# Optimization experiments

Hardware: AMD Instinct MI355X
Metric: run time of the kernel (lower is better)

Reference implementation:

```python
import jax, jax.numpy as jnp
import numpy as np
import math

D_MODEL = 1152
D_K = 1152
NUM_HEADS = 8
HEAD_DIM = D_K // NUM_HEADS  # 144
SIGMA = 2.0
EPS = 1e-6


def rope_2d(keys, positions):
    # keys: [B, N, D]; positions: [B, N, 2] float (x, y)
    B, N, D = keys.shape
    half = D // 2
    quarter = D // 4
    idx = jnp.arange(quarter, dtype=keys.dtype)
    theta = 1.0 / (10000.0 ** (2.0 * idx / half))  # [quarter]
    fx = positions[..., 0][..., None] * theta  # [B, N, quarter]
    fy = positions[..., 1][..., None] * theta

    def apply_rope(part, f):
        p = part.reshape(B, N, quarter, 2)
        c, s = jnp.cos(f), jnp.sin(f)
        o1 = p[..., 0] * c - p[..., 1] * s
        o2 = p[..., 0] * s + p[..., 1] * c
        return jnp.stack([o1, o2], axis=-1).reshape(B, N, half)

    return jnp.concatenate(
        [apply_rope(keys[..., :half], fx), apply_rope(keys[..., half:], fy)], axis=-1
    )


def layernorm_nobias(x, w, eps=EPS):
    mu = jnp.mean(x, axis=-1, keepdims=True)
    var = jnp.mean(jnp.square(x - mu), axis=-1, keepdims=True)
    return (x - mu) * jax.lax.rsqrt(var + eps) * w


def setup_inputs() -> dict:
    key = jax.random.key(0)
    ks = jax.random.split(key, 9)
    T, HW, M = 64, 729, 512
    features = jax.random.normal(ks[0], (T, HW, D_MODEL), dtype=jnp.float32)
    tracks = jax.random.uniform(ks[1], (T, M, 2), dtype=jnp.float32) * 27.0
    track_tokens = jax.random.normal(ks[2], (T, M, D_MODEL), dtype=jnp.float32)
    feature_positions = jax.random.uniform(ks[3], (HW, 2), dtype=jnp.float32) * 27.0
    sc = 1.0 / math.sqrt(D_MODEL)
    # weights stored [in, out]; torch Linear computes x @ W.T with W [out, in]
    W_q = jax.random.normal(ks[4], (D_MODEL, D_K), dtype=jnp.float32) * sc
    W_k = jax.random.normal(ks[5], (D_MODEL, D_K), dtype=jnp.float32) * sc
    q_norm_w = jnp.ones((D_K,), dtype=jnp.float32)
    k_norm_w = jnp.ones((D_K,), dtype=jnp.float32)
    out_proj_w = jax.random.normal(ks[6], (D_MODEL, D_MODEL), dtype=jnp.float32) * sc
    return {
        "features": features,
        "tracks": tracks,
        "track_tokens": track_tokens,
        "feature_positions": feature_positions,
        "W_q": W_q,
        "W_k": W_k,
        "q_norm_w": q_norm_w,
        "k_norm_w": k_norm_w,
        "out_proj_w": out_proj_w,
    }


def reference(features, tracks, track_tokens, feature_positions,
              W_q, W_k, q_norm_w, k_norm_w, out_proj_w):
    T, HW, _ = features.shape
    M = tracks.shape[1]
    Q = track_tokens @ W_q  # [T, M, d_k]
    K = features @ W_k      # [T, HW, d_k]
    feat_pos = jnp.broadcast_to(feature_positions[None], (T, HW, 2))
    K = rope_2d(K, feat_pos)
    Q = layernorm_nobias(Q, q_norm_w)
    K = layernorm_nobias(K, k_norm_w)
    Qh = Q.reshape(T, M, NUM_HEADS, HEAD_DIM).transpose(0, 2, 1, 3)   # [T,H,M,dh]
    Kh = K.reshape(T, HW, NUM_HEADS, HEAD_DIM).transpose(0, 2, 1, 3)  # [T,H,HW,dh]
    Vh = features.reshape(T, HW, NUM_HEADS, -1).transpose(0, 2, 1, 3) # [T,H,HW,dv]
    scores = jnp.einsum("thmd,thnd->thmn", Qh, Kh) / math.sqrt(HEAD_DIM)
    # Gaussian spatial bias: -||track - feat||^2 / (2 sigma^2), shared across heads
    diff = tracks[:, :, None, :] - feature_positions[None, None, :, :]  # [T,M,HW,2]
    dist2 = jnp.sum(jnp.square(diff), axis=-1)  # [T,M,HW]
    bias = -dist2 / (2.0 * SIGMA ** 2)
    scores = scores + bias[:, None, :, :]
    attn = jax.nn.softmax(scores, axis=-1)
    sampled = jnp.einsum("thmn,thnd->thmd", attn, Vh)  # [T,H,M,dv]
    sampled = sampled.transpose(0, 2, 1, 3).reshape(T, M, -1)
    return sampled @ out_proj_w
```

## Files before the change

kernel.cpp:

```cpp
#include <hip/hip_runtime.h>
#include <hip/hip_bf16.h>
#include <math.h>

typedef float f32x4 __attribute__((ext_vector_type(4)));
typedef __bf16 bf16x8 __attribute__((ext_vector_type(8)));

#define T_N 64
#define HW_N 729
#define HW_P 736
#define M_N 512
#define DM 1152
#define NH 8
#define DH 144
#define MQ 32768
#define MK 46656
#define MK_PAD 46720

#define SZ_FEAT ((size_t)MK_PAD * DM * 2)
#define SZ_VT   ((size_t)T_N * NH * DH * HW_P * 2)
#define SZ_OV   (SZ_VT > SZ_FEAT ? SZ_VT : SZ_FEAT)
#define SZ_Q    ((size_t)MQ * DM * 2)
#define SZ_W    ((size_t)DM * DM * 2)
#define OFF_KN   ((size_t)0)
#define OFF_TOK  (OFF_KN + SZ_FEAT)
#define OFF_QN   (OFF_TOK + SZ_Q)
#define OFF_OV   (OFF_QN + SZ_Q)
#define OFF_WT   (OFF_OV + SZ_OV)
#define WS_NEED  (OFF_WT + 3 * SZ_W)

__device__ __forceinline__ void async_copy16(void* lds, const void* g) {
    __builtin_amdgcn_global_load_lds(
        (const __attribute__((address_space(1))) void*)g,
        (__attribute__((address_space(3))) void*)lds, 16, 0, 0);
}

__global__ __launch_bounds__(256) void cvt_bf16(const float* __restrict__ src,
                                                __bf16* __restrict__ dst,
                                                long valid4, long total4) {
    long i = (long)blockIdx.x * 256 + threadIdx.x;
    if (i >= total4) return;
    float4 f = {0.f, 0.f, 0.f, 0.f};
    if (i < valid4) f = ((const float4*)src)[i];
    __bf16 tmp[4] = {(__bf16)f.x, (__bf16)f.y, (__bf16)f.z, (__bf16)f.w};
    *((uint2*)(dst + i * 4)) = *((uint2*)tmp);
}

__global__ __launch_bounds__(256) void transpose_w(const float* __restrict__ W,
                                                   __bf16* __restrict__ Wt) {
    __shared__ float tile[32][33];
    const int k0 = blockIdx.x * 32, n0 = blockIdx.y * 32;
    const int tx = threadIdx.x, ty = threadIdx.y;
    #pragma unroll
    for (int i = 0; i < 32; i += 8)
        tile[ty + i][tx] = W[(long)(k0 + ty + i) * DM + n0 + tx];
    __syncthreads();
    #pragma unroll
    for (int i = 0; i < 32; i += 8)
        Wt[(long)(n0 + ty + i) * DM + k0 + tx] = (__bf16)tile[tx][ty + i];
}

__global__ __launch_bounds__(256) void transpose_v(const float* __restrict__ f,
                                                   __bf16* __restrict__ vt) {
    __shared__ float tile[32][149];
    const int hw0 = blockIdx.x * 32, h = blockIdx.y, t = blockIdx.z;
    const int tid = threadIdx.x;
    for (int c = tid; c < 32 * 36; c += 256) {
        const int r = c / 36, s = c % 36;
        const int hw = hw0 + r;
        float4 v = {0.f, 0.f, 0.f, 0.f};
        if (hw < HW_N) v = *(const float4*)(f + ((long)t * HW_N + hw) * DM + h * DH + s * 4);
        tile[r][s * 4 + 0] = v.x; tile[r][s * 4 + 1] = v.y;
        tile[r][s * 4 + 2] = v.z; tile[r][s * 4 + 3] = v.w;
    }
    __syncthreads();
    for (int c = tid; c < DH * 4; c += 256) {
        const int d = c >> 2, s = c & 3;
        __bf16 tmp[8];
        #pragma unroll
        for (int i = 0; i < 8; ++i) tmp[i] = (__bf16)tile[s * 8 + i][d];
        *(uint4*)(vt + ((long)(t * NH + h) * DH + d) * HW_P + hw0 + s * 8) = *(uint4*)tmp;
    }
}

template<bool STORE_BF16>
__global__ __launch_bounds__(256) void gemm_bt(const __bf16* __restrict__ A,
                                               const __bf16* __restrict__ Bt,
                                               void* __restrict__ Cout) {
    __shared__ __align__(16) __bf16 As[128 * 32];
    __shared__ __align__(16) __bf16 Bs[128 * 32];
    const int tid  = threadIdx.x;
    const int wave = tid >> 6, lane = tid & 63;
    const int quad = lane >> 4, l16 = lane & 15;
    const int wr = wave >> 1, wc = wave & 1;
    const long m0 = (long)blockIdx.x * 128;
    const long n0 = (long)blockIdx.y * 128;
    const int swzr = quad ^ ((l16 >> 1) & 3);
    f32x4 acc[4][4] = {};
    for (int kt = 0; kt < 36; ++kt) {
        const int k0 = kt * 32;
        __syncthreads();
        #pragma unroll
        for (int s = 0; s < 2; ++s) {
            const int c = s * 256 + tid;
            const int row = c >> 2;
            const int gkc = (c & 3) ^ ((c >> 3) & 3);
            async_copy16(As + c * 8, A  + (m0 + row) * DM + k0 + gkc * 8);
            async_copy16(Bs + c * 8, Bt + (n0 + row) * DM + k0 + gkc * 8);
        }
        __syncthreads();
        bf16x8 af[4], bfr[4];
        #pragma unroll
        for (int i = 0; i < 4; ++i)
            af[i] = *(const bf16x8*)(As + (wr * 64 + i * 16 + l16) * 32 + swzr * 8);
        #pragma unroll
        for (int j = 0; j < 4; ++j)
            bfr[j] = *(const bf16x8*)(Bs + (wc * 64 + j * 16 + l16) * 32 + swzr * 8);
        #pragma unroll
        for (int i = 0; i < 4; ++i)
            #pragma unroll
            for (int j = 0; j < 4; ++j)
                acc[i][j] = __builtin_amdgcn_mfma_f32_16x16x32_bf16(af[i], bfr[j], acc[i][j], 0, 0, 0);
    }
    #pragma unroll
    for (int i = 0; i < 4; ++i) {
        #pragma unroll
        for (int j = 0; j < 4; ++j) {
            #pragma unroll
            for (int r = 0; r < 4; ++r) {
                const long row = m0 + wr * 64 + i * 16 + quad * 4 + r;
                const long col = n0 + wc * 64 + j * 16 + l16;
                if constexpr (STORE_BF16)
                    ((__bf16*)Cout)[row * DM + col] = (__bf16)acc[i][j][r];
                else
                    ((float*)Cout)[row * DM + col] = acc[i][j][r];
            }
        }
    }
}

__global__ __launch_bounds__(256) void ln_q(__bf16* __restrict__ Q, const float* __restrict__ w) {
    const long row = blockIdx.x;
    __bf16* p = Q + row * DM;
    const int tid = threadIdx.x;
    float v[5];
    int nv = 0;
    float s = 0.f, s2 = 0.f;
    for (int i = tid; i < DM; i += 256) {
        float x = (float)p[i];
        v[nv++] = x; s += x; s2 += x * x;
    }
    #pragma unroll
    for (int o = 32; o > 0; o >>= 1) { s += __shfl_down(s, o); s2 += __shfl_down(s2, o); }
    __shared__ float red[8];
    if ((tid & 63) == 0) { red[tid >> 6] = s; red[4 + (tid >> 6)] = s2; }
    __syncthreads();
    const float S  = red[0] + red[1] + red[2] + red[3];
    const float S2 = red[4] + red[5] + red[6] + red[7];
    const float mu  = S * (1.f / DM);
    const float var = S2 * (1.f / DM) - mu * mu;
    const float rstd = rsqrtf(var + 1e-6f);
    nv = 0;
    for (int i = tid; i < DM; i += 256)
        p[i] = (__bf16)((v[nv++] - mu) * rstd * w[i]);
}

__global__ __launch_bounds__(256) void rope_ln_k(__bf16* __restrict__ K,
                                                 const float* __restrict__ fpos,
                                                 const float* __restrict__ w) {
    const long row = blockIdx.x;
    const int hw = (int)(row % HW_N);
    const float px = fpos[hw * 2 + 0];
    const float py = fpos[hw * 2 + 1];
    __bf16* p = K + row * DM;
    __shared__ float buf[DM];
    __shared__ float red[8];
    const int tid = threadIdx.x;
    float s = 0.f, s2 = 0.f;
    for (int pr = tid; pr < 576; pr += 256) {
        const bool isx = pr < 288;
        const int  i   = isx ? pr : pr - 288;
        const int  off = isx ? 2 * i : 576 + 2 * i;
        const float pos = isx ? px : py;
        const float theta = exp2f((float)i * -0.046137890206768924f);
        float sn, cs;
        sincosf(pos * theta, &sn, &cs);
        const float a = (float)p[off], b = (float)p[off + 1];
        const float o1 = a * cs - b * sn;
        const float o2 = a * sn + b * cs;
        buf[off] = o1; buf[off + 1] = o2;
        s += o1 + o2; s2 += o1 * o1 + o2 * o2;
    }
    #pragma unroll
    for (int o = 32; o > 0; o >>= 1) { s += __shfl_down(s, o); s2 += __shfl_down(s2, o); }
    if ((tid & 63) == 0) { red[tid >> 6] = s; red[4 + (tid >> 6)] = s2; }
    __syncthreads();
    const float S  = red[0] + red[1] + red[2] + red[3];
    const float S2 = red[4] + red[5] + red[6] + red[7];
    const float mu  = S * (1.f / DM);
    const float var = S2 * (1.f / DM) - mu * mu;
    const float rstd = rsqrtf(var + 1e-6f);
    for (int i = tid; i < DM; i += 256)
        p[i] = (__bf16)((buf[i] - mu) * rstd * w[i]);
}

__global__ __launch_bounds__(256, 3) void attn(const __bf16* __restrict__ Qn,
                                               const __bf16* __restrict__ Kn,
                                               const __bf16* __restrict__ Vt,
                                               const float* __restrict__ tracks,
                                               const float* __restrict__ fpos,
                                               __bf16* __restrict__ Out) {
    __shared__ __align__(16) __bf16 VtL[DH * 72];
    __shared__ __align__(16) __bf16 Ps[128 * 72];
    __shared__ float2 trkL[128];
    const int b  = blockIdx.x;
    const int qt = b & 3;
    const int th = b >> 2;
    const int h  = th & 7;
    const int t  = th >> 3;
    const int tid = threadIdx.x;
    const int wave = tid >> 6, lane = tid & 63;
    const int quad = lane >> 4, l16 = lane & 15;
    const int wq = wave * 32;

    if (tid < 128) trkL[tid] = ((const float2*)tracks)[(long)t * M_N + qt * 128 + tid];

    const __bf16* qb = Qn + ((long)t * M_N + qt * 128 + wq) * DM + h * DH;
    const __bf16* kb = Kn + (long)t * HW_N * DM + h * DH;
    const __bf16* vb = Vt + (long)(t * NH + h) * DH * HW_P;
    const __bf16* zpg = Kn + (size_t)MK * DM;

    f32x4 Ot[2][9] = {};
    float mrow[2][4], lrow[2][4];
    #pragma unroll
    for (int rt = 0; rt < 2; ++rt)
        #pragma unroll
        for (int r = 0; r < 4; ++r) { mrow[rt][r] = -1e30f; lrow[rt][r] = 0.f; }

    for (int kt = 0; kt < 12; ++kt) {
        const int kv0 = kt * 64;
        __syncthreads();
        for (int c = tid; c < DH * 9; c += 256) {
            const int r = c / 9, s = c % 9;
            const __bf16* g = (s < 8 && (kv0 + s * 8 + 8) <= HW_P)
                                ? vb + (long)r * HW_P + kv0 + s * 8 : zpg;
            async_copy16(VtL + c * 8, g);
        }
        __syncthreads();
        f32x4 sc[2][4] = {};
        #pragma unroll
        for (int kc = 0; kc < 5; ++kc) {
            bf16x8 aq[2];
            #pragma unroll
            for (int rt = 0; rt < 2; ++rt) {
                uint4 u = {0u, 0u, 0u, 0u};
                if (kc < 4 || quad < 2)
                    u = *(const uint4*)(qb + (long)(rt * 16 + l16) * DM + kc * 32 + quad * 8);
                aq[rt] = *(bf16x8*)&u;
            }
            #pragma unroll
            for (int jt = 0; jt < 4; ++jt) {
                const bf16x8 bk = *(const bf16x8*)(kb + (long)(kv0 + jt * 16 + l16) * DM + kc * 32 + quad * 8);
                #pragma unroll
                for (int rt = 0; rt < 2; ++rt)
                    sc[rt][jt] = __builtin_amdgcn_mfma_f32_16x16x32_bf16(aq[rt], bk, sc[rt][jt], 0, 0, 0);
            }
        }
        float fx[4], fy[4]; bool msk[4];
        #pragma unroll
        for (int jt = 0; jt < 4; ++jt) {
            const int kv = kv0 + jt * 16 + l16;
            msk[jt] = kv >= HW_N;
            float2 fp = {0.f, 0.f};
            if (!msk[jt]) fp = ((const float2*)fpos)[kv];
            fx[jt] = fp.x; fy[jt] = fp.y;
        }
        float alpha[2][4];
        #pragma unroll
        for (int rt = 0; rt < 2; ++rt) {
            #pragma unroll
            for (int r = 0; r < 4; ++r) {
                const int row = wq + rt * 16 + quad * 4 + r;
                const float tx = trkL[row].x, ty = trkL[row].y;
                float sv[4];
                float mx = -1e30f;
                #pragma unroll
                for (int jt = 0; jt < 4; ++jt) {
                    const float dx = tx - fx[jt], dy = ty - fy[jt];
                    float v = sc[rt][jt][r] * (1.f / 12.f) - (dx * dx + dy * dy) * 0.125f;
                    if (msk[jt]) v = -1e30f;
                    sv[jt] = v;
                    mx = fmaxf(mx, v);
                }
                #pragma unroll
                for (int o = 1; o < 16; o <<= 1) mx = fmaxf(mx, __shfl_xor(mx, o));
                const float mn = fmaxf(mrow[rt][r], mx);
                const float al = __expf(mrow[rt][r] - mn);
                float rs = 0.f;
                #pragma unroll
                for (int jt = 0; jt < 4; ++jt) {
                    const float p = __expf(sv[jt] - mn);
                    rs += p;
                    Ps[row * 72 + jt * 16 + l16] = (__bf16)p;
                }
                #pragma unroll
                for (int o = 1; o < 16; o <<= 1) rs += __shfl_xor(rs, o);
                lrow[rt][r] = lrow[rt][r] * al + rs;
                mrow[rt][r] = mn;
                alpha[rt][r] = al;
            }
        }
        #pragma unroll
        for (int rt = 0; rt < 2; ++rt)
            #pragma unroll
            for (int d = 0; d < 9; ++d)
                #pragma unroll
                for (int r = 0; r < 4; ++r)
                    Ot[rt][d][r] *= alpha[rt][r];
        __syncthreads();
        #pragma unroll
        for (int kh = 0; kh < 2; ++kh) {
            bf16x8 ap[2];
            #pragma unroll
            for (int rt = 0; rt < 2; ++rt)
                ap[rt] = *(const bf16x8*)(Ps + (wq + rt * 16 + l16) * 72 + kh * 32 + quad * 8);
            #pragma unroll
            for (int d = 0; d < 9; ++d) {
                const bf16x8 bv = *(const bf16x8*)(VtL + (d * 16 + l16) * 72 + kh * 32 + quad * 8);
                #pragma unroll
                for (int rt = 0; rt < 2; ++rt)
                    Ot[rt][d] = __builtin_amdgcn_mfma_f32_16x16x32_bf16(ap[rt], bv, Ot[rt][d], 0, 0, 0);
            }
        }
    }
    #pragma unroll
    for (int rt = 0; rt < 2; ++rt) {
        #pragma unroll
        for (int r = 0; r < 4; ++r) {
            const float inv = 1.f / lrow[rt][r];
            const long row = (long)t * M_N + qt * 128 + wq + rt * 16 + quad * 4 + r;
            #pragma unroll
            for (int d = 0; d < 9; ++d)
                Out[row * DM + h * DH + d * 16 + l16] = (__bf16)(Ot[rt][d][r] * inv);
        }
    }
}

extern "C" void kernel_launch(void* const* d_in, const int* in_sizes, int n_in,
                              void* d_out, int out_size, void* d_ws, size_t ws_size,
                              hipStream_t stream) {
    const float* features = (const float*)d_in[0];
    const float* tracks   = (const float*)d_in[1];
    const float* tok      = (const float*)d_in[2];
    const float* fpos     = (const float*)d_in[3];
    const float* W_q      = (const float*)d_in[4];
    const float* W_k      = (const float*)d_in[5];
    const float* q_w      = (const float*)d_in[6];
    const float* k_w      = (const float*)d_in[7];
    const float* W_o      = (const float*)d_in[8];

    if (ws_size < WS_NEED) return;

    char* ws = (char*)d_ws;
    __bf16* kn      = (__bf16*)(ws + OFF_KN);
    __bf16* tok_bf  = (__bf16*)(ws + OFF_TOK);
    __bf16* qn      = (__bf16*)(ws + OFF_QN);
    __bf16* feat_bf = (__bf16*)(ws + OFF_OV);
    __bf16* vt      = (__bf16*)(ws + OFF_OV);
    __bf16* wt_q    = (__bf16*)(ws + OFF_WT);
    __bf16* wt_k    = (__bf16*)(ws + OFF_WT + SZ_W);
    __bf16* wt_o    = (__bf16*)(ws + OFF_WT + 2 * SZ_W);

    {
        const long valid4 = (long)MK * DM / 4, total4 = (long)MK_PAD * DM / 4;
        cvt_bf16<<<(int)((total4 + 255) / 256), 256, 0, stream>>>(features, feat_bf, valid4, total4);
    }
    {
        const long n4 = (long)MQ * DM / 4;
        cvt_bf16<<<(int)((n4 + 255) / 256), 256, 0, stream>>>(tok, tok_bf, n4, n4);
    }
    dim3 tb(32, 8);
    transpose_w<<<dim3(36, 36), tb, 0, stream>>>(W_q, wt_q);
    transpose_w<<<dim3(36, 36), tb, 0, stream>>>(W_k, wt_k);
    transpose_w<<<dim3(36, 36), tb, 0, stream>>>(W_o, wt_o);

    gemm_bt<true><<<dim3(MQ / 128, DM / 128), 256, 0, stream>>>(tok_bf, wt_q, qn);
    gemm_bt<true><<<dim3(MK_PAD / 128, DM / 128), 256, 0, stream>>>(feat_bf, wt_k, kn);

    ln_q<<<MQ, 256, 0, stream>>>(qn, q_w);
    rope_ln_k<<<MK, 256, 0, stream>>>(kn, fpos, k_w);

    transpose_v<<<dim3(23, NH, T_N), 256, 0, stream>>>(features, vt);

    __bf16* sampled = tok_bf;
    attn<<<T_N * NH * (M_N / 128), 256, 0, stream>>>(qn, kn, vt, tracks, fpos, sampled);

    gemm_bt<false><<<dim3(MQ / 128, DM / 128), 256, 0, stream>>>(sampled, wt_o, d_out);
}
```

Before: 1.741 ms.

## Transpose attention MFMAs to keep P in registers and drop LDS staging

The attention kernel swaps the MFMA operand order so the score tile comes out transposed: each lane holds one query row. That lets softmax reductions use two cross-quad shuffles instead of four. The probabilities then feed the PV MFMA directly from registers, so the Ps LDS buffer and the V LDS staging with its block barriers go away. V is instead read straight from global memory in a permuted layout padded to 768, which the V transpose kernel writes, and block indices are remapped so the four query tiles of one (t,h) share cache. The trade-off is more uncached-path global traffic for V and a dependence on the custom permuted V layout being correct.

```diff
diff --git a/kernel.cpp b/kernel.cpp
--- a/kernel.cpp
+++ b/kernel.cpp
@@ -7,7 +7,7 @@
 
 #define T_N 64
 #define HW_N 729
-#define HW_P 736
+#define HW_PV 768
 #define M_N 512
 #define DM 1152
 #define NH 8
@@ -17,7 +17,7 @@
 #define MK_PAD 46720
 
 #define SZ_FEAT ((size_t)MK_PAD * DM * 2)
-#define SZ_VT   ((size_t)T_N * NH * DH * HW_P * 2)
+#define SZ_VT   ((size_t)T_N * NH * DH * HW_PV * 2)
 #define SZ_OV   (SZ_VT > SZ_FEAT ? SZ_VT : SZ_FEAT)
 #define SZ_Q    ((size_t)MQ * DM * 2)
 #define SZ_W    ((size_t)DM * DM * 2)
@@ -73,12 +73,14 @@
         tile[r][s * 4 + 2] = v.z; tile[r][s * 4 + 3] = v.w;
     }
     __syncthreads();
-    for (int c = tid; c < DH * 4; c += 256) {
-        const int d = c >> 2, s = c & 3;
-        __bf16 tmp[8];
-        #pragma unroll
-        for (int i = 0; i < 8; ++i) tmp[i] = (__bf16)tile[s * 8 + i][d];
-        *(uint4*)(vt + ((long)(t * NH + h) * DH + d) * HW_P + hw0 + s * 8) = *(uint4*)tmp;
+    for (int c = tid; c < DH * 8; c += 256) {
+        const int d = c >> 3, g = c & 7;
+        const int base4 = hw0 + g * 4;
+        const int cb = (base4 & ~31) | (((base4 >> 2) & 3) << 3) | (((base4 >> 4) & 1) << 2);
+        __bf16 tmp[4];
+        #pragma unroll
+        for (int i = 0; i < 4; ++i) tmp[i] = (__bf16)tile[g * 4 + i][d];
+        *(uint2*)(vt + ((long)(t * NH + h) * DH + d) * HW_PV + cb) = *(uint2*)tmp;
     }
 }
 
@@ -209,138 +211,135 @@
                                                const float* __restrict__ tracks,
                                                const float* __restrict__ fpos,
                                                __bf16* __restrict__ Out) {
-    __shared__ __align__(16) __bf16 VtL[DH * 72];
-    __shared__ __align__(16) __bf16 Ps[128 * 72];
-    __shared__ float2 trkL[128];
-    const int b  = blockIdx.x;
-    const int qt = b & 3;
-    const int th = b >> 2;
-    const int h  = th & 7;
-    const int t  = th >> 3;
+    const int i  = blockIdx.x;
+    const int g  = ((i >> 5) << 3) | (i & 7);
+    const int qt = (i >> 3) & 3;
+    const int h  = g & 7, t = g >> 3;
     const int tid = threadIdx.x;
     const int wave = tid >> 6, lane = tid & 63;
     const int quad = lane >> 4, l16 = lane & 15;
     const int wq = wave * 32;
 
-    if (tid < 128) trkL[tid] = ((const float2*)tracks)[(long)t * M_N + qt * 128 + tid];
-
     const __bf16* qb = Qn + ((long)t * M_N + qt * 128 + wq) * DM + h * DH;
     const __bf16* kb = Kn + (long)t * HW_N * DM + h * DH;
-    const __bf16* vb = Vt + (long)(t * NH + h) * DH * HW_P;
-    const __bf16* zpg = Kn + (size_t)MK * DM;
+    const __bf16* vb = Vt + (long)(t * NH + h) * DH * HW_PV;
+
+    float tx[2], ty[2];
+    #pragma unroll
+    for (int rt = 0; rt < 2; ++rt) {
+        const float2 tr = ((const float2*)tracks)[(long)t * M_N + qt * 128 + wq + rt * 16 + l16];
+        tx[rt] = tr.x; ty[rt] = tr.y;
+    }
 
     f32x4 Ot[2][9] = {};
-    float mrow[2][4], lrow[2][4];
-    #pragma unroll
-    for (int rt = 0; rt < 2; ++rt)
-        #pragma unroll
-        for (int r = 0; r < 4; ++r) { mrow[rt][r] = -1e30f; lrow[rt][r] = 0.f; }
+    float mrow[2] = {-1e30f, -1e30f}, lrow[2] = {0.f, 0.f};
 
     for (int kt = 0; kt < 12; ++kt) {
         const int kv0 = kt * 64;
-        __syncthreads();
-        for (int c = tid; c < DH * 9; c += 256) {
-            const int r = c / 9, s = c % 9;
-            const __bf16* g = (s < 8 && (kv0 + s * 8 + 8) <= HW_P)
-                                ? vb + (long)r * HW_P + kv0 + s * 8 : zpg;
-            async_copy16(VtL + c * 8, g);
-        }
-        __syncthreads();
         f32x4 sc[2][4] = {};
         #pragma unroll
         for (int kc = 0; kc < 5; ++kc) {
-            bf16x8 aq[2];
+            bf16x8 bq[2];
             #pragma unroll
             for (int rt = 0; rt < 2; ++rt) {
                 uint4 u = {0u, 0u, 0u, 0u};
                 if (kc < 4 || quad < 2)
                     u = *(const uint4*)(qb + (long)(rt * 16 + l16) * DM + kc * 32 + quad * 8);
-                aq[rt] = *(bf16x8*)&u;
+                bq[rt] = *(bf16x8*)&u;
             }
             #pragma unroll
             for (int jt = 0; jt < 4; ++jt) {
-                const bf16x8 bk = *(const bf16x8*)(kb + (long)(kv0 + jt * 16 + l16) * DM + kc * 32 + quad * 8);
+                const bf16x8 ak = *(const bf16x8*)(kb + (long)(kv0 + jt * 16 + l16) * DM + kc * 32 + quad * 8);
                 #pragma unroll
                 for (int rt = 0; rt < 2; ++rt)
-                    sc[rt][jt] = __builtin_amdgcn_mfma_f32_16x16x32_bf16(aq[rt], bk, sc[rt][jt], 0, 0, 0);
-            }
-        }
-        float fx[4], fy[4]; bool msk[4];
+                    sc[rt][jt] = __builtin_amdgcn_mfma_f32_16x16x32_bf16(ak, bq[rt], sc[rt][jt], 0, 0, 0);
+            }
+        }
         #pragma unroll
         for (int jt = 0; jt < 4; ++jt) {
-            const int kv = kv0 + jt * 16 + l16;
-            msk[jt] = kv >= HW_N;
-            float2 fp = {0.f, 0.f};
-            if (!msk[jt]) fp = ((const float2*)fpos)[kv];
-            fx[jt] = fp.x; fy[jt] = fp.y;
-        }
-        float alpha[2][4];
+            const int kvb = kv0 + jt * 16 + quad * 4;
+            float2 fp[4];
+            if (kvb + 3 < HW_N) {
+                const float4 a  = *(const float4*)(fpos + (long)kvb * 2);
+                const float4 b2 = *(const float4*)(fpos + (long)kvb * 2 + 4);
+                fp[0] = {a.x, a.y};  fp[1] = {a.z, a.w};
+                fp[2] = {b2.x, b2.y}; fp[3] = {b2.z, b2.w};
+            } else {
+                #pragma unroll
+                for (int r = 0; r < 4; ++r) {
+                    const int k2 = (kvb + r < HW_N) ? kvb + r : HW_N - 1;
+                    fp[r] = ((const float2*)fpos)[k2];
+                }
+            }
+            #pragma unroll
+            for (int rt = 0; rt < 2; ++rt)
+                #pragma unroll
+                for (int r = 0; r < 4; ++r) {
+                    const float dx = tx[rt] - fp[r].x, dy = ty[rt] - fp[r].y;
+                    float v = sc[rt][jt][r] * (1.f / 12.f) - (dx * dx + dy * dy) * 0.125f;
+                    if (kvb + r >= HW_N) v = -1e30f;
+                    sc[rt][jt][r] = v;
+                }
+        }
         #pragma unroll
         for (int rt = 0; rt < 2; ++rt) {
-            #pragma unroll
-            for (int r = 0; r < 4; ++r) {
-                const int row = wq + rt * 16 + quad * 4 + r;
-                const float tx = trkL[row].x, ty = trkL[row].y;
-                float sv[4];
-                float mx = -1e30f;
-                #pragma unroll
-                for (int jt = 0; jt < 4; ++jt) {
-                    const float dx = tx - fx[jt], dy = ty - fy[jt];
-                    float v = sc[rt][jt][r] * (1.f / 12.f) - (dx * dx + dy * dy) * 0.125f;
-                    if (msk[jt]) v = -1e30f;
-                    sv[jt] = v;
-                    mx = fmaxf(mx, v);
+            float mp = -1e30f;
+            #pragma unroll
+            for (int jt = 0; jt < 4; ++jt)
+                #pragma unroll
+                for (int r = 0; r < 4; ++r) mp = fmaxf(mp, sc[rt][jt][r]);
+            mp = fmaxf(mp, __shfl_xor(mp, 16));
+            mp = fmaxf(mp, __shfl_xor(mp, 32));
+            const float mn = fmaxf(mrow[rt], mp);
+            const float al = __expf(mrow[rt] - mn);
+            mrow[rt] = mn;
+            float rs = 0.f;
+            #pragma unroll
+            for (int jt = 0; jt < 4; ++jt)
+                #pragma unroll
+                for (int r = 0; r < 4; ++r) {
+                    const float p = __expf(sc[rt][jt][r] - mn);
+                    sc[rt][jt][r] = p;
+                    rs += p;
                 }
-                #pragma unroll
-                for (int o = 1; o < 16; o <<= 1) mx = fmaxf(mx, __shfl_xor(mx, o));
-                const float mn = fmaxf(mrow[rt][r], mx);
-                const float al = __expf(mrow[rt][r] - mn);
-                float rs = 0.f;
-                #pragma unroll
-                for (int jt = 0; jt < 4; ++jt) {
-                    const float p = __expf(sv[jt] - mn);
-                    rs += p;
-                    Ps[row * 72 + jt * 16 + l16] = (__bf16)p;
+            rs += __shfl_xor(rs, 16);
+            rs += __shfl_xor(rs, 32);
+            lrow[rt] = lrow[rt] * al + rs;
+            #pragma unroll
+            for (int d = 0; d < 9; ++d) Ot[rt][d] *= al;
+        }
+        #pragma unroll
+        for (int kh = 0; kh < 2; ++kh) {
+            bf16x8 bp[2];
+            #pragma unroll
+            for (int rt = 0; rt < 2; ++rt) {
+                __bf16 tmp[8];
+                #pragma unroll
+                for (int j = 0; j < 4; ++j) {
+                    tmp[j]     = (__bf16)sc[rt][2 * kh][j];
+                    tmp[4 + j] = (__bf16)sc[rt][2 * kh + 1][j];
                 }
-                #pragma unroll
-                for (int o = 1; o < 16; o <<= 1) rs += __shfl_xor(rs, o);
-                lrow[rt][r] = lrow[rt][r] * al + rs;
-                mrow[rt][r] = mn;
-                alpha[rt][r] = al;
-            }
-        }
-        #pragma unroll
-        for (int rt = 0; rt < 2; ++rt)
-            #pragma unroll
-            for (int d = 0; d < 9; ++d)
-                #pragma unroll
-                for (int r = 0; r < 4; ++r)
-                    Ot[rt][d][r] *= alpha[rt][r];
-        __syncthreads();
-        #pragma unroll
-        for (int kh = 0; kh < 2; ++kh) {
-            bf16x8 ap[2];
-            #pragma unroll
-            for (int rt = 0; rt < 2; ++rt)
-                ap[rt] = *(const bf16x8*)(Ps + (wq + rt * 16 + l16) * 72 + kh * 32 + quad * 8);
-            #pragma unroll
-            for (int d = 0; d < 9; ++d) {
-                const bf16x8 bv = *(const bf16x8*)(VtL + (d * 16 + l16) * 72 + kh * 32 + quad * 8);
+                bp[rt] = *(bf16x8*)tmp;
+            }
+            #pragma unroll
+            for (int dt = 0; dt < 9; ++dt) {
+                const bf16x8 av = *(const bf16x8*)(vb + (long)(dt * 16 + l16) * HW_PV + kv0 + kh * 32 + quad * 8);
                 #pragma unroll
                 for (int rt = 0; rt < 2; ++rt)
-                    Ot[rt][d] = __builtin_amdgcn_mfma_f32_16x16x32_bf16(ap[rt], bv, Ot[rt][d], 0, 0, 0);
+                    Ot[rt][dt] = __builtin_amdgcn_mfma_f32_16x16x32_bf16(av, bp[rt], Ot[rt][dt], 0, 0, 0);
             }
         }
     }
     #pragma unroll
     for (int rt = 0; rt < 2; ++rt) {
-        #pragma unroll
-        for (int r = 0; r < 4; ++r) {
-            const float inv = 1.f / lrow[rt][r];
-            const long row = (long)t * M_N + qt * 128 + wq + rt * 16 + quad * 4 + r;
-            #pragma unroll
-            for (int d = 0; d < 9; ++d)
-                Out[row * DM + h * DH + d * 16 + l16] = (__bf16)(Ot[rt][d][r] * inv);
+        const float inv = 1.f / lrow[rt];
+        const long row = (long)t * M_N + qt * 128 + wq + rt * 16 + l16;
+        #pragma unroll
+        for (int dt = 0; dt < 9; ++dt) {
+            __bf16 o4[4];
+            #pragma unroll
+            for (int r = 0; r < 4; ++r) o4[r] = (__bf16)(Ot[rt][dt][r] * inv);
+            *(uint2*)(Out + row * DM + h * DH + dt * 16 + quad * 4) = *(uint2*)o4;
         }
     }
 }
@@ -389,7 +388,7 @@
     ln_q<<<MQ, 256, 0, stream>>>(qn, q_w);
     rope_ln_k<<<MK, 256, 0, stream>>>(kn, fpos, k_w);
 
-    transpose_v<<<dim3(23, NH, T_N), 256, 0, stream>>>(features, vt);
+    transpose_v<<<dim3(HW_PV / 32, NH, T_N), 256, 0, stream>>>(features, vt);
 
     __bf16* sampled = tok_bf;
     attn<<<T_N * NH * (M_N / 128), 256, 0, stream>>>(qn, kn, vt, tracks, fpos, sampled);
```

Result: slower. 1.994 ms (+14.5%).
